# Optimization experiments

Hardware: AMD Instinct MI355X
Metric: run time of the kernel (lower is better)

Reference implementation:

```python
import jax, jax.numpy as jnp
import numpy as np

N_USERS = 100000
N_ITEMS = 50000
N_NODES = N_USERS + N_ITEMS
N_EDGES = 4800000
EMB_DIM = 64
N_LAYERS = 3


def setup_inputs() -> dict:
    key = jax.random.key(0)
    k1, k2, k3, k4, k5 = jax.random.split(key, 5)
    user_emb = jax.random.normal(k1, (N_USERS, EMB_DIM), dtype=jnp.float32)
    item_emb = jax.random.normal(k2, (N_ITEMS, EMB_DIM), dtype=jnp.float32)
    # COO representation of the (symmetric-normalized) adjacency matrix
    edge_src = jax.random.randint(k3, (N_EDGES,), 0, N_NODES, dtype=jnp.int32)
    edge_dst = jax.random.randint(k4, (N_EDGES,), 0, N_NODES, dtype=jnp.int32)
    edge_weight = jax.random.uniform(k5, (N_EDGES,), dtype=jnp.float32)
    return {
        "user_emb": user_emb,
        "item_emb": item_emb,
        "edge_weight": edge_weight,
        "edge_src": edge_src,
        "edge_dst": edge_dst,
    }


def _spmm(edge_src, edge_dst, edge_weight, x):
    # out[i] = sum_j A[i, j] * x[j]  with A in COO (dst=row i, src=col j)
    msgs = edge_weight[:, None] * x[edge_src]  # [E, D]
    return jax.ops.segment_sum(msgs, edge_dst, num_segments=N_NODES)


def reference(user_emb, item_emb, edge_weight, edge_src, edge_dst):
    ego = jnp.concatenate([user_emb, item_emb], axis=0)  # [N, D]
    acc = ego  # running sum over layer embeddings (layer 0 included)
    for _ in range(N_LAYERS):
        ego = _spmm(edge_src, edge_dst, edge_weight, ego)
        acc = acc + ego
    mean_emb = acc / jnp.float32(N_LAYERS + 1)  # mean over (L+1) layers
    new_user = mean_emb[:N_USERS]
    new_item = mean_emb[N_USERS:]
    return new_user, new_item
```

## Files before the change

### kernel.cpp

```cpp
#include <hip/hip_runtime.h>
#include <hip/hip_fp16.h>

#define N_USERS 100000
#define N_ITEMS 50000
#define N_NODES 150000
#define N_EDGES 4800000
#define EMB 64
#define N_LAYERS 3

#define NBKT 256
#define NPB  586
#define NREP 8
#define SUBCAP 2624
#define CAP (NREP * SUBCAP)

typedef unsigned int u32;
typedef unsigned short u16;
typedef u32 vu4 __attribute__((ext_vector_type(4)));
typedef u32 vu2 __attribute__((ext_vector_type(2)));
typedef float vf4 __attribute__((ext_vector_type(4)));

#define W_BITS 14
#define W_SCALE 16384.0f
#define W_INV   (1.0f / 16384.0f)
#define W_MASK  16383u

__device__ __forceinline__ float hh(u16 v) {
    return __half2float(__ushort_as_half(v));
}

__global__ void k_init(const float4* __restrict__ user,
                       const float4* __restrict__ item,
                       ushort4* __restrict__ cur,
                       int* __restrict__ cursor) {
    int i = blockIdx.x * blockDim.x + threadIdx.x;
    const int total4 = N_NODES * EMB / 4;
    const int user4  = N_USERS * EMB / 4;
    if (i < NREP * NBKT) cursor[i] = 0;
    if (i >= total4) return;
    float4 v = (i < user4) ? user[i] : item[i - user4];
    ushort4 h;
    h.x = __half_as_ushort(__float2half_rn(v.x));
    h.y = __half_as_ushort(__float2half_rn(v.y));
    h.z = __half_as_ushort(__float2half_rn(v.z));
    h.w = __half_as_ushort(__float2half_rn(v.w));
    cur[i] = h;
}

__global__ __launch_bounds__(256) void k_p1(const int4*   __restrict__ src4,
                                            const int4*   __restrict__ dst4,
                                            const float4* __restrict__ w4,
                                            int* __restrict__ cursor,
                                            u32* __restrict__ pk_arr,
                                            u16* __restrict__ ld_arr) {
    __shared__ int hist[NBKT];
    __shared__ int base[NBKT];
    __shared__ int bscan[NBKT];
    __shared__ u32 s_pk[2048];
    __shared__ u32 s_meta[2048];
    int tid = threadIdx.x;
    hist[tid] = 0;
    __syncthreads();

    int g0 = blockIdx.x * 512 + tid * 2;
    bool act = (g0 < N_EDGES / 4);

    u32 pk[8];
    u32 meta[8];
    int rk[8];
    if (act) {
        int4 d0 = dst4[g0], d1 = dst4[g0 + 1];
        int4 s0 = src4[g0], s1 = src4[g0 + 1];
        float4 f0 = w4[g0], f1 = w4[g0 + 1];
        int   ds[8] = {d0.x, d0.y, d0.z, d0.w, d1.x, d1.y, d1.z, d1.w};
        int   ss[8] = {s0.x, s0.y, s0.z, s0.w, s1.x, s1.y, s1.z, s1.w};
        float wf[8] = {f0.x, f0.y, f0.z, f0.w, f1.x, f1.y, f1.z, f1.w};
        #pragma unroll
        for (int k = 0; k < 8; ++k) {
            u32 d  = (u32)ds[k];
            u32 b  = d / NPB;
            u32 ld = d - b * NPB;
            rk[k]  = atomicAdd(&hist[b], 1);
            u32 wq = (u32)(wf[k] * W_SCALE + 0.5f);
            if (wq > W_MASK) wq = W_MASK;
            pk[k]   = ((u32)ss[k] << W_BITS) | wq;
            meta[k] = (b << 10) | ld;
        }
    }
    __syncthreads();

    int rep = blockIdx.x & (NREP - 1);
    int h = hist[tid];
    if (h > 0) base[tid] = atomicAdd(&cursor[rep * NBKT + tid], h);
    bscan[tid] = h;
    __syncthreads();
    for (int off = 1; off < NBKT; off <<= 1) {
        int t = 0;
        if (tid >= off) t = bscan[tid - off];
        __syncthreads();
        if (tid >= off) bscan[tid] += t;
        __syncthreads();
    }

    if (act) {
        #pragma unroll
        for (int k = 0; k < 8; ++k) {
            u32 b = meta[k] >> 10;
            int s = (bscan[b] - hist[b]) + rk[k];
            s_pk[s]   = pk[k];
            s_meta[s] = meta[k];
        }
    }
    __syncthreads();

    int total = bscan[NBKT - 1];
    #pragma unroll
    for (int k = 0; k < 8; ++k) {
        int s = k * 256 + tid;
        if (s < total) {
            u32 mt = s_meta[s];
            u32 b  = mt >> 10;
            int pos = base[b] + (s - (bscan[b] - hist[b]));
            if (pos < SUBCAP) {
                size_t slot = (size_t)b * CAP + (size_t)rep * SUBCAP + pos;
                pk_arr[slot] = s_pk[s];
                ld_arr[slot] = (u16)(mt & 1023u);
            }
        }
    }
}

__global__ __launch_bounds__(1024) void k_p2(const int* __restrict__ cursor,
                                             const u32* __restrict__ pk_arr,
                                             const u16* __restrict__ ld_arr,
                                             int* __restrict__ row_ptr,
                                             u32* __restrict__ pairs) {
    __shared__ int hist[1024];
    __shared__ int cur[NPB];
    __shared__ int btot[NBKT];
    __shared__ int bsum[NBKT];
    int b = blockIdx.x;
    int tid = threadIdx.x;
    hist[tid] = 0;
    if (tid < NBKT) {
        int s = 0;
        #pragma unroll
        for (int r = 0; r < NREP; ++r) s += cursor[r * NBKT + tid];
        btot[tid] = s;
        bsum[tid] = s;
    }
    if (b == 0 && tid == 0) row_ptr[N_NODES] = N_EDGES;
    __syncthreads();
    for (int off = 1; off < NBKT; off <<= 1) {
        int t = 0;
        if (tid < NBKT && tid >= off) t = bsum[tid - off];
        __syncthreads();
        if (tid < NBKT && tid >= off) bsum[tid] += t;
        __syncthreads();
    }
    int gbase = bsum[b] - btot[b];

    int lo = b * NPB;
    int nb = N_NODES - lo; if (nb > NPB) nb = NPB;

    int n[NREP];
    #pragma unroll
    for (int r = 0; r < NREP; ++r) {
        int c = cursor[r * NBKT + b];
        n[r] = (c > SUBCAP) ? SUBCAP : c;
    }

    for (int r = 0; r < NREP; ++r) {
        const u16* p = ld_arr + (size_t)b * CAP + (size_t)r * SUBCAP;
        for (int i = tid; i < n[r]; i += 1024)
            atomicAdd(&hist[p[i]], 1);
    }
    __syncthreads();

    int val = hist[tid];
    for (int off = 1; off < 1024; off <<= 1) {
        int t = 0;
        if (tid >= off) t = hist[tid - off];
        __syncthreads();
        if (tid >= off) hist[tid] += t;
        __syncthreads();
    }
    int excl = hist[tid] - val;
    if (tid < nb) {
        row_ptr[lo + tid] = gbase + excl;
        cur[tid] = excl;
    }
    __syncthreads();

    for (int r = 0; r < NREP; ++r) {
        const u16* p = ld_arr + (size_t)b * CAP + (size_t)r * SUBCAP;
        const u32* q = pk_arr + (size_t)b * CAP + (size_t)r * SUBCAP;
        for (int i = tid; i < n[r]; i += 1024) {
            int ld  = p[i];
            int pos = atomicAdd(&cur[ld], 1);
            pairs[gbase + pos] = q[i];
        }
    }
}

struct Dec4 { u32 r0, r1, r2, r3; float w0, w1, w2, w3; };

__device__ __forceinline__ Dec4 dec_fast(vu4 p) {
    Dec4 d;
    d.r0 = p.x >> W_BITS; d.w0 = (float)(p.x & W_MASK);
    d.r1 = p.y >> W_BITS; d.w1 = (float)(p.y & W_MASK);
    d.r2 = p.z >> W_BITS; d.w2 = (float)(p.z & W_MASK);
    d.r3 = p.w >> W_BITS; d.w3 = (float)(p.w & W_MASK);
    return d;
}

__device__ __forceinline__ Dec4 dec_mask(vu4 p, int eb, int beg, int end) {
    Dec4 d;
    bool v0 = (eb + 0 >= beg) && (eb + 0 < end);
    bool v1 = (eb + 1 >= beg) && (eb + 1 < end);
    bool v2 = (eb + 2 >= beg) && (eb + 2 < end);
    bool v3 = (eb + 3 >= beg) && (eb + 3 < end);
    d.r0 = v0 ? (p.x >> W_BITS) : 0u; d.w0 = v0 ? (float)(p.x & W_MASK) : 0.f;
    d.r1 = v1 ? (p.y >> W_BITS) : 0u; d.w1 = v1 ? (float)(p.y & W_MASK) : 0.f;
    d.r2 = v2 ? (p.z >> W_BITS) : 0u; d.w2 = v2 ? (float)(p.z & W_MASK) : 0.f;
    d.r3 = v3 ? (p.w >> W_BITS) : 0u; d.w3 = v3 ? (float)(p.w & W_MASK) : 0.f;
    return d;
}

__device__ __forceinline__ Dec4 dec(vu4 p, int lo, int beg, int end, int g) {
    if (lo >= beg && lo + 16 <= end) return dec_fast(p);
    return dec_mask(p, lo + 4 * g, beg, end);
}

__device__ __forceinline__ vu4 ldp(const u32* p) {
    return __builtin_nontemporal_load((const vu4*)p);
}

__device__ __forceinline__ vu2 ldx(const char* xbase, u32 r, u32 moff) {
    return *(const vu2*)(xbase + (size_t)(r * 128u + moff));
}

__device__ __forceinline__ void fmix2(float& a0, float& a1, float w, u32 x) {
    asm("v_fma_mix_f32 %0, %1, %2, %0 op_sel:[0,0,0] op_sel_hi:[0,1,0]"
        : "+v"(a0) : "v"(w), "v"(x));
    asm("v_fma_mix_f32 %0, %1, %2, %0 op_sel:[0,1,0] op_sel_hi:[0,1,0]"
        : "+v"(a1) : "v"(w), "v"(x));
}

__device__ __forceinline__ void acc4(vu2 xv, float w,
                                     float& ax, float& ay, float& az, float& aw) {
    fmix2(ax, ay, w, xv.x);
    fmix2(az, aw, w, xv.y);
}

#define LOADX(pfx, d) \
    vu2 pfx##0 = ldx(xbase, d.r0, moff), pfx##1 = ldx(xbase, d.r1, moff), \
        pfx##2 = ldx(xbase, d.r2, moff), pfx##3 = ldx(xbase, d.r3, moff)
#define ACCX(pfx, d) \
    acc4(pfx##0, d.w0, ax, ay, az, aw); acc4(pfx##1, d.w1, ax, ay, az, aw); \
    acc4(pfx##2, d.w2, ax, ay, az, aw); acc4(pfx##3, d.w3, ax, ay, az, aw)
#define RED(v) v += __shfl_xor(v, 16); v += __shfl_xor(v, 32)

template<int FIN>
__global__ __launch_bounds__(256) void k_gather(const int* __restrict__ row_ptr,
                                                const u32* __restrict__ pairs,
                                                const __half* __restrict__ x,
                                                __half* __restrict__ nxt,
                                                const ushort4* __restrict__ e0,
                                                const ushort4* __restrict__ e1,
                                                const ushort4* __restrict__ e2,
                                                float* __restrict__ outp) {
    int wave = (blockIdx.x * blockDim.x + threadIdx.x) >> 6;
    int lane = threadIdx.x & 63;
    if (wave >= N_NODES) return;

    const int m = lane & 15;
    ushort4 ega = {}, ea = {}, eb = {};
    if (FIN && lane < 16) {
        size_t idx = (size_t)wave * 16 + m;
        ega = e0[idx]; ea = e1[idx]; eb = e2[idx];
    }

    int beg = row_ptr[wave];
    int end = row_ptr[wave + 1];

    const int g = lane >> 4;
    const u32 moff = (u32)m << 3;
    const char* xbase = (const char*)x;

    float ax = 0.f, ay = 0.f, az = 0.f, aw = 0.f;

    int jb = beg & ~3;
    int nb = (end - jb + 15) >> 4;
    const u32* pp = pairs + jb + 4 * g;

    if (nb == 1) {
        vu4 P0 = ldp(pp);
        Dec4 d0 = dec(P0, jb, beg, end, g);
        LOADX(xa, d0);
        ACCX(xa, d0);
    } else if (nb == 2) {
        vu4 P0 = ldp(pp);
        vu4 P1 = ldp(pp + 16);
        Dec4 d0 = dec(P0, jb, beg, end, g);
        LOADX(xa, d0);
        Dec4 d1 = dec(P1, jb + 16, beg, end, g);
        LOADX(xc, d1);
        ACCX(xa, d0);
        ACCX(xc, d1);
    } else if (nb == 3) {
        vu4 P0 = ldp(pp);
        vu4 P1 = ldp(pp + 16);
        vu4 P2 = ldp(pp + 32);
        Dec4 d0 = dec(P0, jb, beg, end, g);
        LOADX(xa, d0);
        Dec4 d1 = dec(P1, jb + 16, beg, end, g);
        LOADX(xc, d1);
        ACCX(xa, d0);
        Dec4 d2 = dec(P2, jb + 32, beg, end, g);
        LOADX(xd, d2);
        ACCX(xc, d1);
        ACCX(xd, d2);
    } else if (nb >= 4) {
        vu4 P0 = ldp(pp);
        vu4 P1 = ldp(pp + 16);
        vu4 P2 = ldp(pp + 32);
        Dec4 d0 = dec(P0, jb, beg, end, g);
        LOADX(xa, d0);
        Dec4 d1 = dec(P1, jb + 16, beg, end, g);
        LOADX(xc, d1);
        ACCX(xa, d0);
        vu4 P3 = ldp(pp + 48);
        Dec4 d2 = dec(P2, jb + 32, beg, end, g);
        LOADX(xd, d2);
        ACCX(xc, d1);
        Dec4 d3 = dec(P3, jb + 48, beg, end, g);
        LOADX(xe, d3);
        ACCX(xd, d2);
        ACCX(xe, d3);
        for (int b = 4; b < nb; ++b) {
            vu4 Pl = ldp(pp + (size_t)16 * b);
            Dec4 dl = dec(Pl, jb + 16 * b, beg, end, g);
            LOADX(xf, dl);
            ACCX(xf, dl);
        }
    }

    RED(ax); RED(ay); RED(az); RED(aw);

    if (lane < 16) {
        if (FIN) {
            vf4 o;
            o.x = (hh(ega.x) + hh(ea.x) + hh(eb.x) + ax * W_INV) * 0.25f;
            o.y = (hh(ega.y) + hh(ea.y) + hh(eb.y) + ay * W_INV) * 0.25f;
            o.z = (hh(ega.z) + hh(ea.z) + hh(eb.z) + az * W_INV) * 0.25f;
            o.w = (hh(ega.w) + hh(ea.w) + hh(eb.w) + aw * W_INV) * 0.25f;
            __builtin_nontemporal_store(o, (vf4*)outp + (size_t)wave * 16 + m);
        } else {
            ushort4 h;
            h.x = __half_as_ushort(__float2half_rn(ax * W_INV));
            h.y = __half_as_ushort(__float2half_rn(ay * W_INV));
            h.z = __half_as_ushort(__float2half_rn(az * W_INV));
            h.w = __half_as_ushort(__float2half_rn(aw * W_INV));
            ((ushort4*)nxt)[(size_t)wave * 16 + m] = h;
        }
    }
}

__global__ void k_spmm(const int*   __restrict__ src,
                       const int*   __restrict__ dst,
                       const float* __restrict__ w,
                       const float* __restrict__ x,
                       float*       __restrict__ y) {
    long long t = (long long)blockIdx.x * blockDim.x + threadIdx.x;
    int e = (int)(t >> 4);
    if (e >= N_EDGES) return;
    int q = (int)(t & 15);
    int   s  = src[e];
    int   d  = dst[e];
    float we = w[e];
    const float4* xs = (const float4*)(x + (long long)s * EMB);
    float4 v = xs[q];
    float* yd = y + (long long)d * EMB + q * 4;
    atomicAdd(yd + 0, we * v.x);
    atomicAdd(yd + 1, we * v.y);
    atomicAdd(yd + 2, we * v.z);
    atomicAdd(yd + 3, we * v.w);
}

__global__ void k_init_f32(const float4* __restrict__ user,
                           const float4* __restrict__ item,
                           float4* __restrict__ out,
                           float4* __restrict__ cur) {
    int i = blockIdx.x * blockDim.x + threadIdx.x;
    const int total4 = N_NODES * EMB / 4;
    const int user4  = N_USERS * EMB / 4;
    if (i >= total4) return;
    float4 v = (i < user4) ? user[i] : item[i - user4];
    out[i] = v;
    cur[i] = v;
}

__global__ void k_acc(float4* __restrict__ out,
                      const float4* __restrict__ buf,
                      float scale) {
    int i = blockIdx.x * blockDim.x + threadIdx.x;
    const int total4 = N_NODES * EMB / 4;
    if (i >= total4) return;
    float4 o = out[i];
    float4 b = buf[i];
    o.x = (o.x + b.x) * scale;
    o.y = (o.y + b.y) * scale;
    o.z = (o.z + b.z) * scale;
    o.w = (o.w + b.w) * scale;
    out[i] = o;
}

extern "C" void kernel_launch(void* const* d_in, const int* in_sizes, int n_in,
                              void* d_out, int out_size, void* d_ws, size_t ws_size,
                              hipStream_t stream) {
    const float* user_emb = (const float*)d_in[0];
    const float* item_emb = (const float*)d_in[1];
    const float* edge_w   = (const float*)d_in[2];
    const int*   edge_src = (const int*)d_in[3];
    const int*   edge_dst = (const int*)d_in[4];
    float* out = (float*)d_out;

    const size_t feat_elems = (size_t)N_NODES * EMB;
    const size_t feat_bytes_f32 = feat_elems * 4;
    const size_t feat_bytes_f16 = feat_elems * 2;

    char* ws = (char*)d_ws;
    size_t off = 0;
    __half* h0 = (__half*)(ws + off); off += feat_bytes_f16;
    __half* h1 = (__half*)(ws + off); off += feat_bytes_f16;
    __half* h2 = (__half*)(ws + off); off += feat_bytes_f16;
    int* row_ptr  = (int*)(ws + off); off += ((size_t)(N_NODES + 1) * 4 + 63) / 64 * 64;
    int* cursor   = (int*)(ws + off); off += (size_t)NREP * NBKT * 4;
    u32* pk_arr = (u32*)(ws + off);   off += (size_t)NBKT * CAP * 4;
    u16* ld_arr = (u16*)(ws + off);   off += (size_t)NBKT * CAP * 2;
    u32* pairs  = (u32*)(ws + off);   off += (size_t)N_EDGES * 4 + 64;
    const size_t needed = off;

    const int block = 256;
    const int total4 = (int)(feat_elems / 4);
    const int fgrid = (total4 + block - 1) / block;
    const int p1grid = (N_EDGES / 8 + block - 1) / block;
    const int ggrid = (N_NODES + 3) / 4;

    if (ws_size >= needed) {
        k_init<<<fgrid, block, 0, stream>>>((const float4*)user_emb,
                                            (const float4*)item_emb,
                                            (ushort4*)h0, cursor);

        k_p1<<<p1grid, block, 0, stream>>>((const int4*)edge_src,
                                           (const int4*)edge_dst,
                                           (const float4*)edge_w,
                                           cursor, pk_arr, ld_arr);
        k_p2<<<NBKT, 1024, 0, stream>>>(cursor, pk_arr, ld_arr,
                                        row_ptr, pairs);

        k_gather<0><<<ggrid, block, 0, stream>>>(row_ptr, pairs, h0, h1,
                                                 nullptr, nullptr, nullptr,
                                                 nullptr);
        k_gather<0><<<ggrid, block, 0, stream>>>(row_ptr, pairs, h1, h2,
                                                 nullptr, nullptr, nullptr,
                                                 nullptr);
        k_gather<1><<<ggrid, block, 0, stream>>>(row_ptr, pairs, h2, nullptr,
                                                 (const ushort4*)h0,
                                                 (const ushort4*)h1,
                                                 (const ushort4*)h2,
                                                 out);
    } else {
        float* buf0 = (float*)d_ws;
        float* buf1 = buf0 + feat_elems;
        k_init_f32<<<fgrid, block, 0, stream>>>((const float4*)user_emb,
                                                (const float4*)item_emb,
                                                (float4*)out, (float4*)buf0);
        float* cur = buf0;
        float* nxt = buf1;
        for (int layer = 0; layer < N_LAYERS; ++layer) {
            (void)hipMemsetAsync(nxt, 0, feat_bytes_f32, stream);
            long long threads = (long long)N_EDGES * 16;
            int grid = (int)((threads + block - 1) / block);
            k_spmm<<<grid, block, 0, stream>>>(edge_src, edge_dst, edge_w, cur, nxt);
            float scale = (layer == N_LAYERS - 1) ? (1.0f / (N_LAYERS + 1)) : 1.0f;
            k_acc<<<fgrid, block, 0, stream>>>((float4*)out, (const float4*)nxt, scale);
            float* tmp = cur; cur = nxt; nxt = tmp;
        }
    }
}
```

Measured before the change: 442.4 us.

## Fuse fp16 init into bucket pass and stage CSR scatter through shared memory

The fp16 conversion of the embeddings is folded into the edge-bucketing kernel as extra blocks, and the cursor zeroing moves to a memset, so one launch disappears and the two jobs can overlap. In k_p2 the per-row scatter now writes into a dynamic shared buffer of CAP words (about 84 KB), which is then copied to the global pairs array in contiguous order instead of as scattered global writes. The large shared allocation cuts occupancy of k_p2, and it only fits if the dynamic shared size is allowed by the device.

After: 416.3 us. 5.9% less time.

```diff
diff --git a/kernel.cpp b/kernel.cpp
--- a/kernel.cpp
+++ b/kernel.cpp
@@ -13,6 +13,8 @@
 #define NREP 8
 #define SUBCAP 2624
 #define CAP (NREP * SUBCAP)
+#define P1GRID 2344
+#define INITGRID 9375
 
 typedef unsigned int u32;
 typedef unsigned short u16;
@@ -29,36 +31,37 @@
     return __half2float(__ushort_as_half(v));
 }
 
-__global__ void k_init(const float4* __restrict__ user,
-                       const float4* __restrict__ item,
-                       ushort4* __restrict__ cur,
-                       int* __restrict__ cursor) {
-    int i = blockIdx.x * blockDim.x + threadIdx.x;
-    const int total4 = N_NODES * EMB / 4;
-    const int user4  = N_USERS * EMB / 4;
-    if (i < NREP * NBKT) cursor[i] = 0;
-    if (i >= total4) return;
-    float4 v = (i < user4) ? user[i] : item[i - user4];
-    ushort4 h;
-    h.x = __half_as_ushort(__float2half_rn(v.x));
-    h.y = __half_as_ushort(__float2half_rn(v.y));
-    h.z = __half_as_ushort(__float2half_rn(v.z));
-    h.w = __half_as_ushort(__float2half_rn(v.w));
-    cur[i] = h;
-}
-
-__global__ __launch_bounds__(256) void k_p1(const int4*   __restrict__ src4,
-                                            const int4*   __restrict__ dst4,
-                                            const float4* __restrict__ w4,
-                                            int* __restrict__ cursor,
-                                            u32* __restrict__ pk_arr,
-                                            u16* __restrict__ ld_arr) {
+__global__ __launch_bounds__(256) void k_build1(const int4*   __restrict__ src4,
+                                                const int4*   __restrict__ dst4,
+                                                const float4* __restrict__ w4,
+                                                int* __restrict__ cursor,
+                                                u32* __restrict__ pk_arr,
+                                                u16* __restrict__ ld_arr,
+                                                const float4* __restrict__ user,
+                                                const float4* __restrict__ item,
+                                                ushort4* __restrict__ h0) {
+    int tid = threadIdx.x;
+
+    if (blockIdx.x >= P1GRID) {
+        int i = (int)(blockIdx.x - P1GRID) * 256 + tid;
+        const int total4 = N_NODES * EMB / 4;
+        const int user4  = N_USERS * EMB / 4;
+        if (i >= total4) return;
+        float4 v = (i < user4) ? user[i] : item[i - user4];
+        ushort4 h;
+        h.x = __half_as_ushort(__float2half_rn(v.x));
+        h.y = __half_as_ushort(__float2half_rn(v.y));
+        h.z = __half_as_ushort(__float2half_rn(v.z));
+        h.w = __half_as_ushort(__float2half_rn(v.w));
+        h0[i] = h;
+        return;
+    }
+
     __shared__ int hist[NBKT];
     __shared__ int base[NBKT];
     __shared__ int bscan[NBKT];
     __shared__ u32 s_pk[2048];
     __shared__ u32 s_meta[2048];
-    int tid = threadIdx.x;
     hist[tid] = 0;
     __syncthreads();
 
@@ -130,13 +133,15 @@
     }
 }
 
+extern __shared__ u32 s_pk2[];
+
 __global__ __launch_bounds__(1024) void k_p2(const int* __restrict__ cursor,
                                              const u32* __restrict__ pk_arr,
                                              const u16* __restrict__ ld_arr,
                                              int* __restrict__ row_ptr,
                                              u32* __restrict__ pairs) {
     __shared__ int hist[1024];
-    __shared__ int cur[NPB];
+    __shared__ int start[NPB];
     __shared__ int btot[NBKT];
     __shared__ int bsum[NBKT];
     int b = blockIdx.x;
@@ -161,7 +166,7 @@
     int gbase = bsum[b] - btot[b];
 
     int lo = b * NPB;
-    int nb = N_NODES - lo; if (nb > NPB) nb = NPB;
+    int nbn = N_NODES - lo; if (nbn > NPB) nbn = NPB;
 
     int n[NREP];
     #pragma unroll
@@ -186,21 +191,23 @@
         __syncthreads();
     }
     int excl = hist[tid] - val;
-    if (tid < nb) {
-        row_ptr[lo + tid] = gbase + excl;
-        cur[tid] = excl;
-    }
+    if (tid < nbn) row_ptr[lo + tid] = gbase + excl;
+    if (tid < NPB) start[tid] = excl;
     __syncthreads();
 
     for (int r = 0; r < NREP; ++r) {
         const u16* p = ld_arr + (size_t)b * CAP + (size_t)r * SUBCAP;
         const u32* q = pk_arr + (size_t)b * CAP + (size_t)r * SUBCAP;
         for (int i = tid; i < n[r]; i += 1024) {
-            int ld  = p[i];
-            int pos = atomicAdd(&cur[ld], 1);
-            pairs[gbase + pos] = q[i];
-        }
-    }
+            int slot = atomicAdd(&start[p[i]], 1);
+            s_pk2[slot] = q[i];
+        }
+    }
+    __syncthreads();
+
+    int total = hist[1023];
+    for (int s = tid; s < total; s += 1024)
+        pairs[gbase + s] = s_pk2[s];
 }
 
 struct Dec4 { u32 r0, r1, r2, r3; float w0, w1, w2, w3; };
@@ -445,20 +452,21 @@
     const int block = 256;
     const int total4 = (int)(feat_elems / 4);
     const int fgrid = (total4 + block - 1) / block;
-    const int p1grid = (N_EDGES / 8 + block - 1) / block;
+    const int bgrid = P1GRID + INITGRID;
     const int ggrid = (N_NODES + 3) / 4;
 
     if (ws_size >= needed) {
-        k_init<<<fgrid, block, 0, stream>>>((const float4*)user_emb,
-                                            (const float4*)item_emb,
-                                            (ushort4*)h0, cursor);
-
-        k_p1<<<p1grid, block, 0, stream>>>((const int4*)edge_src,
-                                           (const int4*)edge_dst,
-                                           (const float4*)edge_w,
-                                           cursor, pk_arr, ld_arr);
-        k_p2<<<NBKT, 1024, 0, stream>>>(cursor, pk_arr, ld_arr,
-                                        row_ptr, pairs);
+        (void)hipMemsetAsync(cursor, 0, (size_t)NREP * NBKT * 4, stream);
+
+        k_build1<<<bgrid, block, 0, stream>>>((const int4*)edge_src,
+                                              (const int4*)edge_dst,
+                                              (const float4*)edge_w,
+                                              cursor, pk_arr, ld_arr,
+                                              (const float4*)user_emb,
+                                              (const float4*)item_emb,
+                                              (ushort4*)h0);
+        k_p2<<<NBKT, 1024, (size_t)CAP * 4, stream>>>(cursor, pk_arr, ld_arr,
+                                                      row_ptr, pairs);
 
         k_gather<0><<<ggrid, block, 0, stream>>>(row_ptr, pairs, h0, h1,
                                                  nullptr, nullptr, nullptr,
```
